# Kernel tuning notes

Hardware: AMD Instinct MI355X
Metric: run time of the kernel (lower is better)

Reference implementation:

```python
import jax, jax.numpy as jnp
import numpy as np

B, C, H, W = 4, 256, 64, 64
HID = C // 2


def setup_inputs() -> dict:
    key = jax.random.key(0)
    kx, kp, kt, kg, km = jax.random.split(key, 5)
    return {
        "x": jax.random.normal(kx, (B, C, H, W), dtype=jnp.float32),
        "w_phi": jax.random.normal(kp, (HID, C), dtype=jnp.float32) * 0.02,
        "w_theta": jax.random.normal(kt, (HID, C), dtype=jnp.float32) * 0.02,
        "w_g": jax.random.normal(kg, (HID, C), dtype=jnp.float32) * 0.02,
        "w_mask": jax.random.normal(km, (C, HID), dtype=jnp.float32) * 0.02,
    }


def reference(x, w_phi, w_theta, w_g, w_mask):
    b, c, h, w = x.shape
    n = h * w
    xf = x.reshape(b, c, n)                     # [B,C,N]
    # 1x1 convs == channel GEMMs
    phi = jnp.einsum('oc,bcn->bon', w_phi, xf)      # [B,HID,N]
    theta = jnp.einsum('oc,bcn->bon', w_theta, xf)  # [B,HID,N]
    g = jnp.einsum('oc,bcn->bon', w_g, xf)          # [B,HID,N]
    # attn[b,n,m] = sum_c theta[b,c,n] * phi[b,c,m]   (theta^T @ phi)
    attn = jnp.einsum('bcn,bcm->bnm', theta, phi)   # [B,N,N]
    # Faithful to nn.Softmax(dim=1): normalize over axis 1 (theta index)
    attn = jax.nn.softmax(attn, axis=1)
    # attn_g[b,n,c] = sum_m attn[b,n,m] * g[b,c,m]   (attn @ g^T)
    attn_g = jnp.einsum('bnm,bcm->bcn', attn, g)    # [B,HID,N] (already transposed back)
    mask = jnp.einsum('oc,bcn->bon', w_mask, attn_g).reshape(b, c, h, w)
    return mask + x
```

## Files before the change

kernel.cpp:

```cpp
#include <hip/hip_runtime.h>


#define NB   4
#define CIN  256
#define HIDN 128
#define NPIX 4096

typedef __attribute__((ext_vector_type(8))) short short8;
typedef __attribute__((ext_vector_type(4))) float f32x4;

__device__ __forceinline__ unsigned short f2bf(float f) {
    unsigned u = __builtin_bit_cast(unsigned, f);
    u += 0x7fffu + ((u >> 16) & 1u);
    return (unsigned short)(u >> 16);
}
__device__ __forceinline__ float bf2f(unsigned short s) {
    return __builtin_bit_cast(float, (unsigned)s << 16);
}

__global__ __launch_bounds__(256) void k_proj(
    const float* __restrict__ x,
    const float* __restrict__ w_phi,
    const float* __restrict__ w_theta,
    const float* __restrict__ w_g,
    unsigned short* __restrict__ phiT,
    unsigned short* __restrict__ thetaT,
    unsigned short* __restrict__ gbuf)
{
    const int nt = blockIdx.x, p = blockIdx.y, b = blockIdx.z;
    const int n0 = nt * 128;
    const float* W = (p == 0) ? w_phi : (p == 1) ? w_theta : w_g;
    const float* X = x + (size_t)b * CIN * NPIX;

    __shared__ alignas(16) unsigned short Ws[128][40];
    __shared__ alignas(16) unsigned short Xs[128][40];

    const int tid = threadIdx.x;
    const int wave = tid >> 6, lane = tid & 63;
    const int wm = wave >> 1, wn = wave & 1;
    const int quad = lane >> 4, l16 = lane & 15;

    f32x4 acc[4][4];
#pragma unroll
    for (int i = 0; i < 4; ++i)
#pragma unroll
        for (int j = 0; j < 4; ++j) acc[i][j] = {0.f, 0.f, 0.f, 0.f};

    for (int ks = 0; ks < CIN / 32; ++ks) {
        {
            const int row = tid >> 1, c0 = (tid & 1) * 16;
            const float* src = W + (size_t)row * CIN + ks * 32 + c0;
#pragma unroll
            for (int j = 0; j < 16; ++j) Ws[row][c0 + j] = f2bf(src[j]);
        }
        {
            const int cc = tid >> 3, nn0 = (tid & 7) * 16;
            const float* src = X + (size_t)(ks * 32 + cc) * NPIX + n0 + nn0;
#pragma unroll
            for (int j = 0; j < 16; ++j) Xs[nn0 + j][cc] = f2bf(src[j]);
        }
        __syncthreads();
#pragma unroll
        for (int mi = 0; mi < 4; ++mi) {
            short8 a = *(const short8*)&Ws[wm * 64 + mi * 16 + l16][quad * 8];
#pragma unroll
            for (int ni = 0; ni < 4; ++ni) {
                short8 bb = *(const short8*)&Xs[wn * 64 + ni * 16 + l16][quad * 8];
                acc[mi][ni] = __builtin_amdgcn_mfma_f32_16x16x32_bf16(a, bb, acc[mi][ni], 0, 0, 0);
            }
        }
        __syncthreads();
    }

    if (p < 2) {
        unsigned short* T = (p == 0) ? phiT : thetaT;
#pragma unroll
        for (int mi = 0; mi < 4; ++mi) {
            const int obase = wm * 64 + mi * 16 + quad * 4;
#pragma unroll
            for (int ni = 0; ni < 4; ++ni) {
                const int nn = wn * 64 + ni * 16 + l16;
                uint2 v;
                v.x = (unsigned)f2bf(acc[mi][ni][0]) | ((unsigned)f2bf(acc[mi][ni][1]) << 16);
                v.y = (unsigned)f2bf(acc[mi][ni][2]) | ((unsigned)f2bf(acc[mi][ni][3]) << 16);
                *(uint2*)&T[((size_t)b * NPIX + n0 + nn) * HIDN + obase] = v;
            }
        }
    } else {
#pragma unroll
        for (int mi = 0; mi < 4; ++mi) {
            const int obase = wm * 64 + mi * 16 + quad * 4;
#pragma unroll
            for (int ni = 0; ni < 4; ++ni) {
                const int nn = wn * 64 + ni * 16 + l16;
#pragma unroll
                for (int r = 0; r < 4; ++r)
                    gbuf[((size_t)b * HIDN + obase + r) * NPIX + n0 + nn] = f2bf(acc[mi][ni][r]);
            }
        }
    }
}

__global__ __launch_bounds__(256, 2) void k_colsum(
    const unsigned short* __restrict__ thetaT,
    const unsigned short* __restrict__ phiT,
    float* __restrict__ colsum)
{
    const int mt = blockIdx.x, ntg = blockIdx.y, b = blockIdx.z;
    const int m0 = mt * 128;
    __shared__ alignas(16) unsigned short As[128][136];
    __shared__ alignas(16) unsigned short Bs[128][136];
    const int tid = threadIdx.x;
    const int wave = tid >> 6, lane = tid & 63;
    const int wm = wave >> 1, wn = wave & 1;
    const int quad = lane >> 4, l16 = lane & 15;

#pragma unroll
    for (int i = 0; i < 8; ++i) {
        const int idx = i * 256 + tid;
        const int row = idx >> 4, cc = (idx & 15) * 8;
        *(uint4*)&Bs[row][cc] =
            *(const uint4*)&phiT[((size_t)b * NPIX + m0 + row) * HIDN + cc];
    }

    float csum[4] = {0.f, 0.f, 0.f, 0.f};

    for (int nc = 0; nc < 4; ++nc) {
        const int n0 = ntg * 512 + nc * 128;
        __syncthreads();
#pragma unroll
        for (int i = 0; i < 8; ++i) {
            const int idx = i * 256 + tid;
            const int row = idx >> 4, cc = (idx & 15) * 8;
            *(uint4*)&As[row][cc] =
                *(const uint4*)&thetaT[((size_t)b * NPIX + n0 + row) * HIDN + cc];
        }
        __syncthreads();

        f32x4 acc[4][4];
#pragma unroll
        for (int i = 0; i < 4; ++i)
#pragma unroll
            for (int j = 0; j < 4; ++j) acc[i][j] = {0.f, 0.f, 0.f, 0.f};

#pragma unroll
        for (int ks = 0; ks < 4; ++ks) {
            short8 af[4], bf[4];
#pragma unroll
            for (int mi = 0; mi < 4; ++mi)
                af[mi] = *(const short8*)&As[wm * 64 + mi * 16 + l16][ks * 32 + quad * 8];
#pragma unroll
            for (int ni = 0; ni < 4; ++ni)
                bf[ni] = *(const short8*)&Bs[wn * 64 + ni * 16 + l16][ks * 32 + quad * 8];
#pragma unroll
            for (int mi = 0; mi < 4; ++mi)
#pragma unroll
                for (int ni = 0; ni < 4; ++ni)
                    acc[mi][ni] = __builtin_amdgcn_mfma_f32_16x16x32_bf16(af[mi], bf[ni], acc[mi][ni], 0, 0, 0);
        }
#pragma unroll
        for (int ni = 0; ni < 4; ++ni)
#pragma unroll
            for (int mi = 0; mi < 4; ++mi)
#pragma unroll
                for (int r = 0; r < 4; ++r) csum[ni] += __expf(acc[mi][ni][r]);
    }

#pragma unroll
    for (int ni = 0; ni < 4; ++ni) {
        float s = csum[ni];
        s += __shfl_xor(s, 16);
        s += __shfl_xor(s, 32);
        if (quad == 0)
            atomicAdd(&colsum[(size_t)b * NPIX + m0 + wn * 64 + ni * 16 + l16], s);
    }
}

__global__ void k_zero(float* __restrict__ p) { p[blockIdx.x * 256 + threadIdx.x] = 0.f; }
__global__ void k_zero4(float* __restrict__ p) {
    const size_t i = (size_t)(blockIdx.x * 256 + threadIdx.x) * 4;
    *(f32x4*)&p[i] = f32x4{0.f, 0.f, 0.f, 0.f};
}

__global__ __launch_bounds__(256) void k_scale_g(
    unsigned short* __restrict__ gbuf, const float* __restrict__ colsum)
{
    const int idx = blockIdx.x * 256 + threadIdx.x;
    const int row = idx >> 9;
    const int m0 = (idx & 511) * 8;
    const int b = row >> 7;
    uint4 v = *(uint4*)&gbuf[(size_t)row * NPIX + m0];
    float4 c0 = *(const float4*)&colsum[(size_t)b * NPIX + m0];
    float4 c1 = *(const float4*)&colsum[(size_t)b * NPIX + m0 + 4];
    unsigned short* vs = (unsigned short*)&v;
    const float cs[8] = {c0.x, c0.y, c0.z, c0.w, c1.x, c1.y, c1.z, c1.w};
#pragma unroll
    for (int j = 0; j < 8; ++j) vs[j] = f2bf(bf2f(vs[j]) / cs[j]);
    *(uint4*)&gbuf[(size_t)row * NPIX + m0] = v;
}

__global__ __launch_bounds__(256, 3) void k_attn(
    const unsigned short* __restrict__ thetaT,
    const unsigned short* __restrict__ phiT,
    const unsigned short* __restrict__ gbuf,
    float* __restrict__ O32)
{
    const int nt = blockIdx.x, ms = blockIdx.y, b = blockIdx.z;
    const int n0 = nt * 64;
    const int mstart = ms ? (21 * ms + 1) : 0;
    const int mcount = ms ? 21 : 22;

    __shared__ alignas(16) unsigned short Bs[64][136];
    __shared__ alignas(16) unsigned short Gs[128][72];
    __shared__ alignas(16) unsigned short Ps[64][72];

    const int tid = threadIdx.x;
    const int wave = tid >> 6, lane = tid & 63;
    const int wm = wave >> 1, wn = wave & 1;
    const int quad = lane >> 4, l16 = lane & 15;

    short8 afrag[2][4];
#pragma unroll
    for (int mi = 0; mi < 2; ++mi) {
        const unsigned short* src =
            thetaT + ((size_t)b * NPIX + n0 + wm * 32 + mi * 16 + l16) * HIDN + quad * 8;
#pragma unroll
        for (int ks = 0; ks < 4; ++ks) afrag[mi][ks] = *(const short8*)(src + ks * 32);
    }

    f32x4 accO[2][4];
#pragma unroll
    for (int i = 0; i < 2; ++i)
#pragma unroll
        for (int j = 0; j < 4; ++j) accO[i][j] = {0.f, 0.f, 0.f, 0.f};

    for (int mc = 0; mc < mcount; ++mc) {
        const int m0 = (mstart + mc) * 64;
        __syncthreads();
#pragma unroll
        for (int j = 0; j < 4; ++j) {
            const int idx = j * 256 + tid;
            const int row = idx >> 4, cc = (idx & 15) * 8;
            *(uint4*)&Bs[row][cc] =
                *(const uint4*)&phiT[((size_t)b * NPIX + m0 + row) * HIDN + cc];
        }
#pragma unroll
        for (int j = 0; j < 4; ++j) {
            const int idx = j * 256 + tid;
            const int row = idx >> 3, cc = (idx & 7) * 8;
            *(uint4*)&Gs[row][cc] =
                *(const uint4*)&gbuf[((size_t)b * HIDN + row) * NPIX + m0 + cc];
        }
        __syncthreads();

        f32x4 accS[2][2];
#pragma unroll
        for (int i = 0; i < 2; ++i)
#pragma unroll
            for (int j = 0; j < 2; ++j) accS[i][j] = {0.f, 0.f, 0.f, 0.f};

#pragma unroll
        for (int ks = 0; ks < 4; ++ks) {
            short8 bf[2];
#pragma unroll
            for (int ni = 0; ni < 2; ++ni)
                bf[ni] = *(const short8*)&Bs[wn * 32 + ni * 16 + l16][ks * 32 + quad * 8];
#pragma unroll
            for (int mi = 0; mi < 2; ++mi)
#pragma unroll
                for (int ni = 0; ni < 2; ++ni)
                    accS[mi][ni] = __builtin_amdgcn_mfma_f32_16x16x32_bf16(
                        afrag[mi][ks], bf[ni], accS[mi][ni], 0, 0, 0);
        }
#pragma unroll
        for (int ni = 0; ni < 2; ++ni) {
            const int mcol = wn * 32 + ni * 16 + l16;
#pragma unroll
            for (int mi = 0; mi < 2; ++mi)
#pragma unroll
                for (int r = 0; r < 4; ++r)
                    Ps[wm * 32 + mi * 16 + quad * 4 + r][mcol] = f2bf(__expf(accS[mi][ni][r]));
        }
        __syncthreads();
#pragma unroll
        for (int ks = 0; ks < 2; ++ks) {
            short8 pa[2], gb[4];
#pragma unroll
            for (int mi = 0; mi < 2; ++mi)
                pa[mi] = *(const short8*)&Ps[wm * 32 + mi * 16 + l16][ks * 32 + quad * 8];
#pragma unroll
            for (int ni = 0; ni < 4; ++ni)
                gb[ni] = *(const short8*)&Gs[wn * 64 + ni * 16 + l16][ks * 32 + quad * 8];
#pragma unroll
            for (int mi = 0; mi < 2; ++mi)
#pragma unroll
                for (int ni = 0; ni < 4; ++ni)
                    accO[mi][ni] = __builtin_amdgcn_mfma_f32_16x16x32_bf16(
                        pa[mi], gb[ni], accO[mi][ni], 0, 0, 0);
        }
    }

#pragma unroll
    for (int mi = 0; mi < 2; ++mi)
#pragma unroll
        for (int ni = 0; ni < 4; ++ni)
#pragma unroll
            for (int r = 0; r < 4; ++r) {
                const int nrow = n0 + wm * 32 + mi * 16 + quad * 4 + r;
                const int ccol = wn * 64 + ni * 16 + l16;
                atomicAdd(&O32[((size_t)b * NPIX + nrow) * HIDN + ccol], accO[mi][ni][r]);
            }
}

__global__ __launch_bounds__(256) void k_mask(
    const float* __restrict__ w_mask,
    const float* __restrict__ O32,
    const float* __restrict__ x,
    float* __restrict__ out)
{
    const int nt = blockIdx.x, ct = blockIdx.y, b = blockIdx.z;
    const int n0 = nt * 128, c0 = ct * 128;
    __shared__ alignas(16) unsigned short As[128][40];
    __shared__ alignas(16) unsigned short Bs[128][40];
    const int tid = threadIdx.x;
    const int wave = tid >> 6, lane = tid & 63;
    const int wm = wave >> 1, wn = wave & 1;
    const int quad = lane >> 4, l16 = lane & 15;

    f32x4 acc[4][4];
#pragma unroll
    for (int i = 0; i < 4; ++i)
#pragma unroll
        for (int j = 0; j < 4; ++j) acc[i][j] = {0.f, 0.f, 0.f, 0.f};

    for (int ks = 0; ks < 4; ++ks) {
        {
            const int row = tid >> 1, cc0 = (tid & 1) * 16;
            const float* src = w_mask + (size_t)(c0 + row) * HIDN + ks * 32 + cc0;
#pragma unroll
            for (int j = 0; j < 16; ++j) As[row][cc0 + j] = f2bf(src[j]);
        }
        {
            const int row = tid >> 1, h0 = (tid & 1) * 16;
            const float* src = O32 + ((size_t)b * NPIX + n0 + row) * HIDN + ks * 32 + h0;
#pragma unroll
            for (int j = 0; j < 16; ++j) Bs[row][h0 + j] = f2bf(src[j]);
        }
        __syncthreads();
#pragma unroll
        for (int mi = 0; mi < 4; ++mi) {
            short8 a = *(const short8*)&As[wm * 64 + mi * 16 + l16][quad * 8];
#pragma unroll
            for (int ni = 0; ni < 4; ++ni) {
                short8 bb = *(const short8*)&Bs[wn * 64 + ni * 16 + l16][quad * 8];
                acc[mi][ni] = __builtin_amdgcn_mfma_f32_16x16x32_bf16(a, bb, acc[mi][ni], 0, 0, 0);
            }
        }
        __syncthreads();
    }

#pragma unroll
    for (int mi = 0; mi < 4; ++mi)
#pragma unroll
        for (int ni = 0; ni < 4; ++ni)
#pragma unroll
            for (int r = 0; r < 4; ++r) {
                const int co = c0 + wm * 64 + mi * 16 + quad * 4 + r;
                const int nn = n0 + wn * 64 + ni * 16 + l16;
                const size_t idx = ((size_t)b * CIN + co) * NPIX + nn;
                out[idx] = acc[mi][ni][r] + x[idx];
            }
}

extern "C" void kernel_launch(void* const* d_in, const int* in_sizes, int n_in,
                              void* d_out, int out_size, void* d_ws, size_t ws_size,
                              hipStream_t stream)
{
    (void)in_sizes; (void)n_in; (void)out_size; (void)ws_size;
    const float* x       = (const float*)d_in[0];
    const float* w_phi   = (const float*)d_in[1];
    const float* w_theta = (const float*)d_in[2];
    const float* w_g     = (const float*)d_in[3];
    const float* w_mask  = (const float*)d_in[4];
    float* out = (float*)d_out;

    char* ws = (char*)d_ws;
    unsigned short* phiT   = (unsigned short*)(ws);
    unsigned short* thetaT = (unsigned short*)(ws + 4194304);
    unsigned short* gbuf   = (unsigned short*)(ws + 8388608);
    float*          colsum = (float*)(ws + 12582912);
    float*          O32    = (float*)(ws + 12648448);

    k_proj   <<<dim3(32, 3, 4), 256, 0, stream>>>(x, w_phi, w_theta, w_g, phiT, thetaT, gbuf);
    k_zero   <<<dim3(64),       256, 0, stream>>>(colsum);
    k_zero4  <<<dim3(2048),     256, 0, stream>>>(O32);
    k_colsum <<<dim3(32, 8, 4), 256, 0, stream>>>(thetaT, phiT, colsum);
    k_scale_g<<<dim3(1024),     256, 0, stream>>>(gbuf, colsum);
    k_attn   <<<dim3(64, 3, 4), 256, 0, stream>>>(thetaT, phiT, gbuf, O32);
    k_mask   <<<dim3(32, 2, 4), 256, 0, stream>>>(w_mask, O32, x, out);
}
```

Measured before the change: 200.5 us.

## Swizzle bf16 intermediates, use direct-to-LDS loads and 32x32 MFMA in attention

The projection kernel now writes phiT/thetaT and g in an XOR-swizzled column order, so later kernels can copy tiles straight into unpadded LDS with global_load_lds and still read them without bank conflicts. k_scale_g is adjusted to the swizzled g layout. The attention kernel is restructured to 128-wide m chunks, 32x32x16 MFMAs, a 2-way m split instead of 3, and fewer blocks per SM, which reduces atomics and per-chunk overhead. The f32-to-bf16 packing in the proj and mask loaders is also paired. The price is more LDS per block, lower occupancy, and index math that is easy to get wrong.

```diff
diff --git a/kernel.cpp b/kernel.cpp
--- a/kernel.cpp
+++ b/kernel.cpp
@@ -8,14 +8,23 @@
 
 typedef __attribute__((ext_vector_type(8))) short short8;
 typedef __attribute__((ext_vector_type(4))) float f32x4;
+typedef __attribute__((ext_vector_type(16))) float f32x16;
 
 __device__ __forceinline__ unsigned short f2bf(float f) {
     unsigned u = __builtin_bit_cast(unsigned, f);
     u += 0x7fffu + ((u >> 16) & 1u);
     return (unsigned short)(u >> 16);
 }
+__device__ __forceinline__ unsigned f2bf2(float lo, float hi) {
+    return (unsigned)f2bf(lo) | ((unsigned)f2bf(hi) << 16);
+}
 __device__ __forceinline__ float bf2f(unsigned short s) {
     return __builtin_bit_cast(float, (unsigned)s << 16);
+}
+__device__ __forceinline__ void cp16(void* lds, const void* g) {
+    __builtin_amdgcn_global_load_lds(
+        (const __attribute__((address_space(1))) unsigned int*)g,
+        (__attribute__((address_space(3))) unsigned int*)lds, 16, 0, 0);
 }
 
 __global__ __launch_bounds__(256) void k_proj(
@@ -50,14 +59,17 @@
         {
             const int row = tid >> 1, c0 = (tid & 1) * 16;
             const float* src = W + (size_t)row * CIN + ks * 32 + c0;
-#pragma unroll
-            for (int j = 0; j < 16; ++j) Ws[row][c0 + j] = f2bf(src[j]);
-        }
-        {
-            const int cc = tid >> 3, nn0 = (tid & 7) * 16;
-            const float* src = X + (size_t)(ks * 32 + cc) * NPIX + n0 + nn0;
-#pragma unroll
-            for (int j = 0; j < 16; ++j) Xs[nn0 + j][cc] = f2bf(src[j]);
+            unsigned* dst = (unsigned*)&Ws[row][c0];
+#pragma unroll
+            for (int j = 0; j < 8; ++j) dst[j] = f2bf2(src[2 * j], src[2 * j + 1]);
+        }
+        {
+            const int cp = (tid >> 4) * 2, nn0 = (tid & 15) * 8;
+            const float* s0 = X + (size_t)(ks * 32 + cp) * NPIX + n0 + nn0;
+            const float* s1 = s0 + NPIX;
+#pragma unroll
+            for (int j = 0; j < 8; ++j)
+                *(unsigned*)&Xs[nn0 + j][cp] = f2bf2(s0[j], s1[j]);
         }
         __syncthreads();
 #pragma unroll
@@ -80,10 +92,11 @@
 #pragma unroll
             for (int ni = 0; ni < 4; ++ni) {
                 const int nn = wn * 64 + ni * 16 + l16;
+                const int scol = (((obase >> 3) ^ (nn & 15)) << 3) | (obase & 7);
                 uint2 v;
-                v.x = (unsigned)f2bf(acc[mi][ni][0]) | ((unsigned)f2bf(acc[mi][ni][1]) << 16);
-                v.y = (unsigned)f2bf(acc[mi][ni][2]) | ((unsigned)f2bf(acc[mi][ni][3]) << 16);
-                *(uint2*)&T[((size_t)b * NPIX + n0 + nn) * HIDN + obase] = v;
+                v.x = f2bf2(acc[mi][ni][0], acc[mi][ni][1]);
+                v.y = f2bf2(acc[mi][ni][2], acc[mi][ni][3]);
+                *(uint2*)&T[((size_t)b * NPIX + n0 + nn) * HIDN + scol] = v;
             }
         }
     } else {
@@ -94,8 +107,11 @@
             for (int ni = 0; ni < 4; ++ni) {
                 const int nn = wn * 64 + ni * 16 + l16;
 #pragma unroll
-                for (int r = 0; r < 4; ++r)
-                    gbuf[((size_t)b * HIDN + obase + r) * NPIX + n0 + nn] = f2bf(acc[mi][ni][r]);
+                for (int r = 0; r < 4; ++r) {
+                    const int c = obase + r;
+                    const int scol = n0 + ((((nn >> 3) ^ (c & 15)) << 3) | (nn & 7));
+                    gbuf[((size_t)b * HIDN + c) * NPIX + scol] = f2bf(acc[mi][ni][r]);
+                }
             }
         }
     }
@@ -108,19 +124,20 @@
 {
     const int mt = blockIdx.x, ntg = blockIdx.y, b = blockIdx.z;
     const int m0 = mt * 128;
-    __shared__ alignas(16) unsigned short As[128][136];
-    __shared__ alignas(16) unsigned short Bs[128][136];
+    __shared__ alignas(16) unsigned short As[128][128];
+    __shared__ alignas(16) unsigned short Bs[128][128];
     const int tid = threadIdx.x;
     const int wave = tid >> 6, lane = tid & 63;
     const int wm = wave >> 1, wn = wave & 1;
     const int quad = lane >> 4, l16 = lane & 15;
 
-#pragma unroll
-    for (int i = 0; i < 8; ++i) {
-        const int idx = i * 256 + tid;
-        const int row = idx >> 4, cc = (idx & 15) * 8;
-        *(uint4*)&Bs[row][cc] =
-            *(const uint4*)&phiT[((size_t)b * NPIX + m0 + row) * HIDN + cc];
+    {
+        const unsigned short* src = phiT + ((size_t)b * NPIX + m0) * HIDN;
+#pragma unroll
+        for (int i = 0; i < 8; ++i) {
+            const int u = i * 256 + tid;
+            cp16(&Bs[0][0] + u * 8, src + u * 8);
+        }
     }
 
     float csum[4] = {0.f, 0.f, 0.f, 0.f};
@@ -128,12 +145,13 @@
     for (int nc = 0; nc < 4; ++nc) {
         const int n0 = ntg * 512 + nc * 128;
         __syncthreads();
-#pragma unroll
-        for (int i = 0; i < 8; ++i) {
-            const int idx = i * 256 + tid;
-            const int row = idx >> 4, cc = (idx & 15) * 8;
-            *(uint4*)&As[row][cc] =
-                *(const uint4*)&thetaT[((size_t)b * NPIX + n0 + row) * HIDN + cc];
+        {
+            const unsigned short* src = thetaT + ((size_t)b * NPIX + n0) * HIDN;
+#pragma unroll
+            for (int i = 0; i < 8; ++i) {
+                const int u = i * 256 + tid;
+                cp16(&As[0][0] + u * 8, src + u * 8);
+            }
         }
         __syncthreads();
 
@@ -145,13 +163,14 @@
 
 #pragma unroll
         for (int ks = 0; ks < 4; ++ks) {
+            const int sc = (((ks * 4 + quad) ^ l16) << 3);
             short8 af[4], bf[4];
 #pragma unroll
             for (int mi = 0; mi < 4; ++mi)
-                af[mi] = *(const short8*)&As[wm * 64 + mi * 16 + l16][ks * 32 + quad * 8];
+                af[mi] = *(const short8*)&As[wm * 64 + mi * 16 + l16][sc];
 #pragma unroll
             for (int ni = 0; ni < 4; ++ni)
-                bf[ni] = *(const short8*)&Bs[wn * 64 + ni * 16 + l16][ks * 32 + quad * 8];
+                bf[ni] = *(const short8*)&Bs[wn * 64 + ni * 16 + l16][sc];
 #pragma unroll
             for (int mi = 0; mi < 4; ++mi)
 #pragma unroll
@@ -187,19 +206,20 @@
 {
     const int idx = blockIdx.x * 256 + threadIdx.x;
     const int row = idx >> 9;
-    const int m0 = (idx & 511) * 8;
-    const int b = row >> 7;
-    uint4 v = *(uint4*)&gbuf[(size_t)row * NPIX + m0];
-    float4 c0 = *(const float4*)&colsum[(size_t)b * NPIX + m0];
-    float4 c1 = *(const float4*)&colsum[(size_t)b * NPIX + m0 + 4];
+    const int sc = (idx & 511) * 8;
+    const int bb = row >> 7;
+    const int mt = (sc & ~127) | ((((sc >> 3) & 15) ^ (row & 15)) << 3);
+    uint4 v = *(uint4*)&gbuf[(size_t)row * NPIX + sc];
+    float4 c0 = *(const float4*)&colsum[(size_t)bb * NPIX + mt];
+    float4 c1 = *(const float4*)&colsum[(size_t)bb * NPIX + mt + 4];
     unsigned short* vs = (unsigned short*)&v;
     const float cs[8] = {c0.x, c0.y, c0.z, c0.w, c1.x, c1.y, c1.z, c1.w};
 #pragma unroll
     for (int j = 0; j < 8; ++j) vs[j] = f2bf(bf2f(vs[j]) / cs[j]);
-    *(uint4*)&gbuf[(size_t)row * NPIX + m0] = v;
-}
-
-__global__ __launch_bounds__(256, 3) void k_attn(
+    *(uint4*)&gbuf[(size_t)row * NPIX + sc] = v;
+}
+
+__global__ __launch_bounds__(256, 2) void k_attn(
     const unsigned short* __restrict__ thetaT,
     const unsigned short* __restrict__ phiT,
     const unsigned short* __restrict__ gbuf,
@@ -207,109 +227,97 @@
 {
     const int nt = blockIdx.x, ms = blockIdx.y, b = blockIdx.z;
     const int n0 = nt * 64;
-    const int mstart = ms ? (21 * ms + 1) : 0;
-    const int mcount = ms ? 21 : 22;
-
-    __shared__ alignas(16) unsigned short Bs[64][136];
-    __shared__ alignas(16) unsigned short Gs[128][72];
-    __shared__ alignas(16) unsigned short Ps[64][72];
+
+    __shared__ alignas(16) unsigned short Bs[128][128];
+    __shared__ alignas(16) unsigned short Gs[128][128];
+    __shared__ alignas(16) unsigned short Ps[64][128];
 
     const int tid = threadIdx.x;
     const int wave = tid >> 6, lane = tid & 63;
     const int wm = wave >> 1, wn = wave & 1;
-    const int quad = lane >> 4, l16 = lane & 15;
-
-    short8 afrag[2][4];
-#pragma unroll
-    for (int mi = 0; mi < 2; ++mi) {
-        const unsigned short* src =
-            thetaT + ((size_t)b * NPIX + n0 + wm * 32 + mi * 16 + l16) * HIDN + quad * 8;
-#pragma unroll
-        for (int ks = 0; ks < 4; ++ks) afrag[mi][ks] = *(const short8*)(src + ks * 32);
-    }
-
-    f32x4 accO[2][4];
-#pragma unroll
-    for (int i = 0; i < 2; ++i)
-#pragma unroll
-        for (int j = 0; j < 4; ++j) accO[i][j] = {0.f, 0.f, 0.f, 0.f};
-
-    for (int mc = 0; mc < mcount; ++mc) {
-        const int m0 = (mstart + mc) * 64;
-        __syncthreads();
-#pragma unroll
-        for (int j = 0; j < 4; ++j) {
-            const int idx = j * 256 + tid;
-            const int row = idx >> 4, cc = (idx & 15) * 8;
-            *(uint4*)&Bs[row][cc] =
-                *(const uint4*)&phiT[((size_t)b * NPIX + m0 + row) * HIDN + cc];
-        }
-#pragma unroll
-        for (int j = 0; j < 4; ++j) {
-            const int idx = j * 256 + tid;
-            const int row = idx >> 3, cc = (idx & 7) * 8;
-            *(uint4*)&Gs[row][cc] =
-                *(const uint4*)&gbuf[((size_t)b * HIDN + row) * NPIX + m0 + cc];
-        }
-        __syncthreads();
-
-        f32x4 accS[2][2];
-#pragma unroll
-        for (int i = 0; i < 2; ++i)
-#pragma unroll
-            for (int j = 0; j < 2; ++j) accS[i][j] = {0.f, 0.f, 0.f, 0.f};
-
-#pragma unroll
-        for (int ks = 0; ks < 4; ++ks) {
-            short8 bf[2];
-#pragma unroll
-            for (int ni = 0; ni < 2; ++ni)
-                bf[ni] = *(const short8*)&Bs[wn * 32 + ni * 16 + l16][ks * 32 + quad * 8];
-#pragma unroll
-            for (int mi = 0; mi < 2; ++mi)
-#pragma unroll
-                for (int ni = 0; ni < 2; ++ni)
-                    accS[mi][ni] = __builtin_amdgcn_mfma_f32_16x16x32_bf16(
-                        afrag[mi][ks], bf[ni], accS[mi][ni], 0, 0, 0);
+    const int l31 = lane & 31, lh = lane >> 5;
+    const int key = l31 & 15;
+
+    short8 afrag[8];
+    {
+        const int n = n0 + wm * 32 + l31;
+        const unsigned short* src = thetaT + ((size_t)b * NPIX + n) * HIDN;
+#pragma unroll
+        for (int ks = 0; ks < 8; ++ks)
+            afrag[ks] = *(const short8*)(src + (((ks * 2 + lh) ^ key) << 3));
+    }
+
+    f32x16 accO[2];
+#pragma unroll
+    for (int r = 0; r < 16; ++r) { accO[0][r] = 0.f; accO[1][r] = 0.f; }
+
+    for (int mc = 0; mc < 16; ++mc) {
+        const int m0 = (ms * 16 + mc) * 128;
+        __syncthreads();
+        {
+            const unsigned short* src = phiT + ((size_t)b * NPIX + m0) * HIDN;
+#pragma unroll
+            for (int i = 0; i < 8; ++i) {
+                const int u = i * 256 + tid;
+                cp16(&Bs[0][0] + u * 8, src + u * 8);
+            }
+        }
+        {
+#pragma unroll
+            for (int i = 0; i < 8; ++i) {
+                const int u = i * 256 + tid;
+                const int row = u >> 4, un = u & 15;
+                cp16(&Gs[0][0] + u * 8,
+                     gbuf + ((size_t)b * HIDN + row) * NPIX + m0 + un * 8);
+            }
+        }
+        __syncthreads();
+
+        f32x16 accS[2];
+#pragma unroll
+        for (int r = 0; r < 16; ++r) { accS[0][r] = 0.f; accS[1][r] = 0.f; }
+#pragma unroll
+        for (int ks = 0; ks < 8; ++ks) {
+            const int sc = ((ks * 2 + lh) ^ key) << 3;
+            short8 b0 = *(const short8*)&Bs[wn * 64 + l31][sc];
+            short8 b1 = *(const short8*)&Bs[wn * 64 + 32 + l31][sc];
+            accS[0] = __builtin_amdgcn_mfma_f32_32x32x16_bf16(afrag[ks], b0, accS[0], 0, 0, 0);
+            accS[1] = __builtin_amdgcn_mfma_f32_32x32x16_bf16(afrag[ks], b1, accS[1], 0, 0, 0);
         }
 #pragma unroll
         for (int ni = 0; ni < 2; ++ni) {
-            const int mcol = wn * 32 + ni * 16 + l16;
-#pragma unroll
-            for (int mi = 0; mi < 2; ++mi)
-#pragma unroll
-                for (int r = 0; r < 4; ++r)
-                    Ps[wm * 32 + mi * 16 + quad * 4 + r][mcol] = f2bf(__expf(accS[mi][ni][r]));
-        }
-        __syncthreads();
-#pragma unroll
-        for (int ks = 0; ks < 2; ++ks) {
-            short8 pa[2], gb[4];
-#pragma unroll
-            for (int mi = 0; mi < 2; ++mi)
-                pa[mi] = *(const short8*)&Ps[wm * 32 + mi * 16 + l16][ks * 32 + quad * 8];
-#pragma unroll
-            for (int ni = 0; ni < 4; ++ni)
-                gb[ni] = *(const short8*)&Gs[wn * 64 + ni * 16 + l16][ks * 32 + quad * 8];
-#pragma unroll
-            for (int mi = 0; mi < 2; ++mi)
-#pragma unroll
-                for (int ni = 0; ni < 4; ++ni)
-                    accO[mi][ni] = __builtin_amdgcn_mfma_f32_16x16x32_bf16(
-                        pa[mi], gb[ni], accO[mi][ni], 0, 0, 0);
-        }
-    }
-
-#pragma unroll
-    for (int mi = 0; mi < 2; ++mi)
-#pragma unroll
-        for (int ni = 0; ni < 4; ++ni)
-#pragma unroll
-            for (int r = 0; r < 4; ++r) {
-                const int nrow = n0 + wm * 32 + mi * 16 + quad * 4 + r;
-                const int ccol = wn * 64 + ni * 16 + l16;
-                atomicAdd(&O32[((size_t)b * NPIX + nrow) * HIDN + ccol], accO[mi][ni][r]);
-            }
+            const int m_loc = wn * 64 + ni * 32 + l31;
+#pragma unroll
+            for (int r = 0; r < 16; ++r) {
+                const int n_loc = wm * 32 + (r & 3) + 8 * (r >> 2) + 4 * lh;
+                const int scol = (((m_loc >> 3) ^ (n_loc & 15)) << 3) | (m_loc & 7);
+                Ps[n_loc][scol] = f2bf(__expf(accS[ni][r]));
+            }
+        }
+        __syncthreads();
+        {
+            const int prow = wm * 32 + l31;
+            const int pkey = prow & 15;
+#pragma unroll
+            for (int ks = 0; ks < 8; ++ks) {
+                const int sc = ((ks * 2 + lh) ^ key) << 3;
+                short8 pa = *(const short8*)&Ps[prow][((ks * 2 + lh) ^ pkey) << 3];
+                short8 g0 = *(const short8*)&Gs[wn * 64 + l31][sc];
+                short8 g1 = *(const short8*)&Gs[wn * 64 + 32 + l31][sc];
+                accO[0] = __builtin_amdgcn_mfma_f32_32x32x16_bf16(pa, g0, accO[0], 0, 0, 0);
+                accO[1] = __builtin_amdgcn_mfma_f32_32x32x16_bf16(pa, g1, accO[1], 0, 0, 0);
+            }
+        }
+    }
+
+#pragma unroll
+    for (int ni = 0; ni < 2; ++ni)
+#pragma unroll
+        for (int r = 0; r < 16; ++r) {
+            const int n = n0 + wm * 32 + (r & 3) + 8 * (r >> 2) + 4 * lh;
+            const int c = wn * 64 + ni * 32 + l31;
+            atomicAdd(&O32[((size_t)b * NPIX + n) * HIDN + c], accO[ni][r]);
+        }
 }
 
 __global__ __launch_bounds__(256) void k_mask(
@@ -337,14 +345,16 @@
         {
             const int row = tid >> 1, cc0 = (tid & 1) * 16;
             const float* src = w_mask + (size_t)(c0 + row) * HIDN + ks * 32 + cc0;
-#pragma unroll
-            for (int j = 0; j < 16; ++j) As[row][cc0 + j] = f2bf(src[j]);
+            unsigned* dst = (unsigned*)&As[row][cc0];
+#pragma unroll
+            for (int j = 0; j < 8; ++j) dst[j] = f2bf2(src[2 * j], src[2 * j + 1]);
         }
         {
             const int row = tid >> 1, h0 = (tid & 1) * 16;
             const float* src = O32 + ((size_t)b * NPIX + n0 + row) * HIDN + ks * 32 + h0;
-#pragma unroll
-            for (int j = 0; j < 16; ++j) Bs[row][h0 + j] = f2bf(src[j]);
+            unsigned* dst = (unsigned*)&Bs[row][h0];
+#pragma unroll
+            for (int j = 0; j < 8; ++j) dst[j] = f2bf2(src[2 * j], src[2 * j + 1]);
         }
         __syncthreads();
 #pragma unroll
@@ -396,6 +406,6 @@
     k_zero4  <<<dim3(2048),     256, 0, stream>>>(O32);
     k_colsum <<<dim3(32, 8, 4), 256, 0, stream>>>(thetaT, phiT, colsum);
     k_scale_g<<<dim3(1024),     256, 0, stream>>>(gbuf, colsum);
-    k_attn   <<<dim3(64, 3, 4), 256, 0, stream>>>(thetaT, phiT, gbuf, O32);
+    k_attn   <<<dim3(64, 2, 4), 256, 0, stream>>>(thetaT, phiT, gbuf, O32);
     k_mask   <<<dim3(32, 2, 4), 256, 0, stream>>>(w_mask, O32, x, out);
 }
```

After: 186.5 us. 7.0% less time.
